# Kernel optimization log

Hardware: AMD Instinct MI355X
Metric: run time of the kernel (lower is better)

The kernel has to match this reference:

```python
import jax, jax.numpy as jnp
from jax import lax
import numpy as np

INPUT_SIZE = 300
HIDDEN = 128
NUM_CLASSES = 2
BATCH = 256
SEQ = 512


def setup_inputs() -> dict:
    key = jax.random.key(0)
    ks = jax.random.split(key, 7)
    s = 1.0 / np.sqrt(HIDDEN)
    x = jax.random.normal(ks[0], (BATCH, SEQ, INPUT_SIZE), dtype=jnp.float32)
    # PyTorch GRU parameter layout: gates stacked [reset; update; new] along dim 0
    W_ih = jax.random.uniform(ks[1], (3 * HIDDEN, INPUT_SIZE), jnp.float32, -s, s)
    W_hh = jax.random.uniform(ks[2], (3 * HIDDEN, HIDDEN), jnp.float32, -s, s)
    b_ih = jax.random.uniform(ks[3], (3 * HIDDEN,), jnp.float32, -s, s)
    b_hh = jax.random.uniform(ks[4], (3 * HIDDEN,), jnp.float32, -s, s)
    W_out = jax.random.uniform(ks[5], (NUM_CLASSES, HIDDEN), jnp.float32, -s, s)
    b_out = jax.random.uniform(ks[6], (NUM_CLASSES,), jnp.float32, -s, s)
    return {"x": x, "W_ih": W_ih, "W_hh": W_hh, "b_ih": b_ih,
            "b_hh": b_hh, "W_out": W_out, "b_out": b_out}


def reference(x, W_ih, W_hh, b_ih, b_hh, W_out, b_out):
    B, T, _ = x.shape
    H = W_hh.shape[1]
    # Precompute input-to-gate projections for all timesteps: [B, T, 3H]
    xg = jnp.einsum('bti,gi->btg', x, W_ih) + b_ih
    xg_t = jnp.swapaxes(xg, 0, 1)  # [T, B, 3H]

    def step(h, xg_step):
        hg = h @ W_hh.T + b_hh                                  # [B, 3H]
        r = jax.nn.sigmoid(xg_step[:, :H] + hg[:, :H])
        z = jax.nn.sigmoid(xg_step[:, H:2 * H] + hg[:, H:2 * H])
        n = jnp.tanh(xg_step[:, 2 * H:] + r * hg[:, 2 * H:])
        h_new = (1.0 - z) * n + z * h
        return h_new, None

    h0 = jnp.zeros((B, H), dtype=x.dtype)
    h_last, _ = lax.scan(step, h0, xg_t)
    # forward takes GRU output at last timestep -> relu -> linear -> log_softmax
    feat = jax.nn.relu(h_last)
    logits = feat @ W_out.T + b_out
    return jax.nn.log_softmax(logits, axis=1)
```

## Files before the change

### kernel.cpp

```cpp
#include <hip/hip_runtime.h>
#include <hip/hip_bf16.h>
#include <math.h>

#define BATCH 256
#define SEQ   512
#define INS   300
#define KP    320
#define HID   128
#define NG    384

typedef __attribute__((ext_vector_type(8))) short short8;
typedef __attribute__((ext_vector_type(4))) float f32x4;

__device__ __forceinline__ float bf2f(unsigned short u) {
    unsigned int v = ((unsigned int)u) << 16;
    return __uint_as_float(v);
}
__device__ __forceinline__ unsigned short f2bf(float f) {
    unsigned int u = __float_as_uint(f);
    unsigned int r = (u + 0x7FFFu + ((u >> 16) & 1u)) >> 16;
    return (unsigned short)r;
}

__global__ void conv_wih(const float* __restrict__ Wih,
                         unsigned short* __restrict__ Whi,
                         unsigned short* __restrict__ Wlo)
{
    int idx = blockIdx.x * 256 + threadIdx.x;
    if (idx >= NG * KP) return;
    int g = idx / KP, k = idx - g * KP;
    float v = (k < INS) ? Wih[g * INS + k] : 0.f;
    unsigned short h = f2bf(v);
    float r = v - bf2f(h);
    Whi[idx] = h;
    Wlo[idx] = f2bf(r);
}

template <bool BF16OUT>
__launch_bounds__(512, 2)
__global__ void xg_fused(const float* __restrict__ x,
                         const unsigned short* __restrict__ Whi,
                         const unsigned short* __restrict__ Wlo,
                         const float* __restrict__ bih,
                         void* __restrict__ xg_out,
                         int t0, int CT)
{
    __shared__ unsigned short Ah[128][40], Al[128][40];

    const int tid  = threadIdx.x;
    const int lane = tid & 63;
    const int w    = tid >> 6;
    const int wm   = (w & 1) * 64;
    const int wn   = (w >> 1) * 96;
    const int m0   = blockIdx.x * 128;

    const int srow = tid >> 2;
    const int kq   = tid & 3;
    const int rr = m0 + srow;
    const int bb = rr / CT;
    const float* xrow = x + (size_t)(bb * SEQ + t0 + (rr - bb * CT)) * INS;

    const int lmf = lane & 15;
    const int lk  = (lane >> 4) * 8;

    f32x4 acc[4][6] = {};

    float av[8];
    auto loadA = [&](int ks) {
        const int k0 = ks * 32 + kq * 8;
        if (k0 + 8 <= INS) {
            float4 f0 = *(const float4*)(xrow + k0);
            float4 f1 = *(const float4*)(xrow + k0 + 4);
            av[0] = f0.x; av[1] = f0.y; av[2] = f0.z; av[3] = f0.w;
            av[4] = f1.x; av[5] = f1.y; av[6] = f1.z; av[7] = f1.w;
        } else {
            #pragma unroll
            for (int i = 0; i < 8; i++)
                av[i] = (k0 + i < INS) ? xrow[k0 + i] : 0.f;
        }
    };
    loadA(0);

    for (int ks = 0; ks < KP / 32; ks++) {
        short8 bh[6], bl[6];
        #pragma unroll
        for (int ni = 0; ni < 6; ni++) {
            const size_t off = (size_t)(wn + ni * 16 + lmf) * KP + ks * 32 + lk;
            bh[ni] = *(const short8*)(Whi + off);
            bl[ni] = *(const short8*)(Wlo + off);
        }

        __syncthreads();
        {
            union { unsigned short us[8]; uint4 q; } ph, pl;
            #pragma unroll
            for (int i = 0; i < 8; i++) {
                unsigned short h = f2bf(av[i]);
                ph.us[i] = h;
                pl.us[i] = f2bf(av[i] - bf2f(h));
            }
            *(uint4*)&Ah[srow][kq * 8] = ph.q;
            *(uint4*)&Al[srow][kq * 8] = pl.q;
        }
        if (ks + 1 < KP / 32) loadA(ks + 1);
        __syncthreads();

        short8 ah[4], al[4];
        #pragma unroll
        for (int mi = 0; mi < 4; mi++) {
            ah[mi] = *(const short8*)&Ah[wm + mi * 16 + lmf][lk];
            al[mi] = *(const short8*)&Al[wm + mi * 16 + lmf][lk];
        }
        #pragma unroll
        for (int ni = 0; ni < 6; ni++) {
            #pragma unroll
            for (int mi = 0; mi < 4; mi++) {
                acc[mi][ni] = __builtin_amdgcn_mfma_f32_16x16x32_bf16(ah[mi], bh[ni], acc[mi][ni], 0, 0, 0);
                acc[mi][ni] = __builtin_amdgcn_mfma_f32_16x16x32_bf16(ah[mi], bl[ni], acc[mi][ni], 0, 0, 0);
                acc[mi][ni] = __builtin_amdgcn_mfma_f32_16x16x32_bf16(al[mi], bh[ni], acc[mi][ni], 0, 0, 0);
            }
        }
    }

    const int crow = (lane >> 4) * 4;
    #pragma unroll
    for (int ni = 0; ni < 6; ni++) {
        const int col = wn + ni * 16 + lmf;
        const float bias = bih[col];
        #pragma unroll
        for (int mi = 0; mi < 4; mi++) {
            #pragma unroll
            for (int i = 0; i < 4; i++) {
                const size_t row = (size_t)(m0 + wm + mi * 16 + crow + i);
                const float val = acc[mi][ni][i] + bias;
                if (BF16OUT) ((unsigned short*)xg_out)[row * NG + col] = f2bf(val);
                else         ((float*)xg_out)[row * NG + col] = val;
            }
        }
    }
}

template <bool BF16XG>
__launch_bounds__(512, 2)
__global__ void gru_mfma(const void* __restrict__ xg_in,
                         const float* __restrict__ Whh,
                         const float* __restrict__ bhh,
                         float* __restrict__ hstate,
                         int t0, int CT, int initial, int final_chunk,
                         const float* __restrict__ Wout,
                         const float* __restrict__ bout,
                         float* __restrict__ out)
{
    const int b    = blockIdx.x;
    const int tid  = threadIdx.x;
    const int w    = tid >> 6;
    const int lane = tid & 63;
    const int lm   = lane & 15;
    const int quad = lane >> 4;

    __shared__ alignas(16) unsigned short hbuf[2][2][160];
    __shared__ float red[2 * HID];

    const int mts[3] = {w, 8 + w, 16 + w};

    short8 w_hi[3][4], w_lo[3][4];
    #pragma unroll
    for (int t = 0; t < 3; t++) {
        const float* wrow = Whh + (size_t)(mts[t] * 16 + lm) * HID + quad * 8;
        #pragma unroll
        for (int kt = 0; kt < 4; kt++) {
            float4 f0 = *(const float4*)(wrow + kt * 32);
            float4 f1 = *(const float4*)(wrow + kt * 32 + 4);
            float vv[8] = {f0.x, f0.y, f0.z, f0.w, f1.x, f1.y, f1.z, f1.w};
            short8 h8, l8;
            #pragma unroll
            for (int i = 0; i < 8; i++) {
                unsigned short h = f2bf(vv[i]);
                h8[i] = (short)h;
                l8[i] = (short)f2bf(vv[i] - bf2f(h));
            }
            w_hi[t][kt] = h8;
            w_lo[t][kt] = l8;
        }
    }

    const int jd = w * 16 + lm;
    float hprev = 0.f, bhr = 0.f, bhz = 0.f, bhn = 0.f, wo0 = 0.f, wo1 = 0.f;
    float nx0r = 0.f, nx0z = 0.f, nx0n = 0.f;
    float nx1r = 0.f, nx1z = 0.f, nx1n = 0.f;
    const float* xgf = (const float*)xg_in;
    const unsigned short* xgb = (const unsigned short*)xg_in;

    if (lane < 16) {
        float h0 = initial ? 0.f : hstate[b * HID + jd];
        hprev = h0;
        bhr = bhh[jd]; bhz = bhh[HID + jd]; bhn = bhh[2 * HID + jd];
        wo0 = Wout[jd]; wo1 = Wout[HID + jd];
        unsigned short hh = f2bf(h0);
        hbuf[0][0][jd] = hh;
        hbuf[0][1][jd] = f2bf(h0 - bf2f(hh));
        const size_t nb0 = (size_t)b * CT * NG;
        const size_t nb1 = nb0 + NG;
        if (BF16XG) {
            nx0r = bf2f(xgb[nb0 + jd]); nx0z = bf2f(xgb[nb0 + HID + jd]); nx0n = bf2f(xgb[nb0 + 2 * HID + jd]);
            nx1r = bf2f(xgb[nb1 + jd]); nx1z = bf2f(xgb[nb1 + HID + jd]); nx1n = bf2f(xgb[nb1 + 2 * HID + jd]);
        } else {
            nx0r = xgf[nb0 + jd]; nx0z = xgf[nb0 + HID + jd]; nx0n = xgf[nb0 + 2 * HID + jd];
            nx1r = xgf[nb1 + jd]; nx1z = xgf[nb1 + HID + jd]; nx1n = xgf[nb1 + 2 * HID + jd];
        }
    }
    __syncthreads();

    const int psel = ((lm & 3) == 1) ? 1 : 0;

    const f32x4 z4 = {0.f, 0.f, 0.f, 0.f};

#define GRU_STEP(P, T, NXR, NXZ, NXN)                                                             \
    {                                                                                             \
        short8 a2[4];                                                                             \
        _Pragma("unroll")                                                                         \
        for (int kt = 0; kt < 4; kt++)                                                            \
            a2[kt] = *(const short8*)&hbuf[P][psel][kt * 32 + quad * 8];                          \
        f32x4 acc[3];                                                                             \
        _Pragma("unroll")                                                                         \
        for (int t = 0; t < 3; t++)                                                               \
            acc[t] = __builtin_amdgcn_mfma_f32_16x16x32_bf16(a2[0], w_hi[t][0], z4, 0, 0, 0);     \
        _Pragma("unroll")                                                                         \
        for (int kt = 1; kt < 4; kt++) {                                                          \
            _Pragma("unroll")                                                                     \
            for (int t = 0; t < 3; t++)                                                           \
                acc[t] = __builtin_amdgcn_mfma_f32_16x16x32_bf16(a2[kt], w_hi[t][kt], acc[t], 0, 0, 0); \
        }                                                                                         \
        _Pragma("unroll")                                                                         \
        for (int kt = 0; kt < 4; kt++) {                                                          \
            _Pragma("unroll")                                                                     \
            for (int t = 0; t < 3; t++)                                                           \
                acc[t] = __builtin_amdgcn_mfma_f32_16x16x32_bf16(a2[kt], w_lo[t][kt], acc[t], 0, 0, 0); \
        }                                                                                         \
        if (lane < 16) {                                                                          \
                             \
            float hgr = (acc[0][0] + acc[0][1]) + bhr;                                            \
            float hgz = (acc[1][0] + acc[1][1]) + bhz;                                            \
            float hgn = (acc[2][0] + acc[2][1]) + bhn;                                            \
            float rg = __builtin_amdgcn_rcpf(1.f + __expf(-((NXR) + hgr)));                       \
            float zg = __builtin_amdgcn_rcpf(1.f + __expf(-((NXZ) + hgz)));                       \
            float nv = (NXN) + rg * hgn;                                                          \
            float e  = __expf(2.f * nv);                                                          \
            float ng = 1.f - 2.f * __builtin_amdgcn_rcpf(e + 1.f);                                \
            hprev = (1.f - zg) * ng + zg * hprev;                                                 \
            unsigned short hh = f2bf(hprev);                                                      \
            hbuf[1 - (P)][0][jd] = hh;                                                            \
            hbuf[1 - (P)][1][jd] = f2bf(hprev - bf2f(hh));                                        \
            if ((T) + 2 < CT) {         \
                const size_t nb = ((size_t)b * CT + (T) + 2) * NG;                                \
                if (BF16XG) { NXR = bf2f(xgb[nb + jd]); NXZ = bf2f(xgb[nb + HID + jd]); NXN = bf2f(xgb[nb + 2 * HID + jd]); } \
                else        { NXR = xgf[nb + jd];       NXZ = xgf[nb + HID + jd];       NXN = xgf[nb + 2 * HID + jd]; }       \
            }                                                                                     \
        }                                                                                         \
        asm volatile("s_waitcnt lgkmcnt(0)\ns_barrier" ::: "memory");                             \
    }

    for (int tt = 0; tt < CT; tt += 2) {
        GRU_STEP(0, tt,     nx0r, nx0z, nx0n)
        GRU_STEP(1, tt + 1, nx1r, nx1z, nx1n)
    }
#undef GRU_STEP

    if (lane < 16) hstate[b * HID + jd] = hprev;

    if (final_chunk) {
        if (lane < 16) {
            float f = hprev > 0.f ? hprev : 0.f;
            red[jd] = f * wo0;
            red[HID + jd] = f * wo1;
        }
        __syncthreads();
        if (tid < 64) {
            float l0 = red[tid] + red[64 + tid];
            float l1 = red[HID + tid] + red[HID + 64 + tid];
            #pragma unroll
            for (int d = 32; d > 0; d >>= 1) {
                l0 += __shfl_down(l0, d, 64);
                l1 += __shfl_down(l1, d, 64);
            }
            if (tid == 0) {
                l0 += bout[0]; l1 += bout[1];
                float m = fmaxf(l0, l1);
                float lse = m + logf(__expf(l0 - m) + __expf(l1 - m));
                out[b * 2 + 0] = l0 - lse;
                out[b * 2 + 1] = l1 - lse;
            }
        }
    }
}

extern "C" void kernel_launch(void* const* d_in, const int* in_sizes, int n_in,
                              void* d_out, int out_size, void* d_ws, size_t ws_size,
                              hipStream_t stream) {
    const float* x    = (const float*)d_in[0];
    const float* Wih  = (const float*)d_in[1];
    const float* Whh  = (const float*)d_in[2];
    const float* bih  = (const float*)d_in[3];
    const float* bhh  = (const float*)d_in[4];
    const float* Wout = (const float*)d_in[5];
    const float* bout = (const float*)d_in[6];
    float* out = (float*)d_out;

    unsigned short* Whi = (unsigned short*)d_ws;
    unsigned short* Wlo = (unsigned short*)((char*)d_ws + 245760);
    float* hstate = (float*)((char*)d_ws + 491520);
    void*  xg     = (void*)((char*)d_ws + 622592);
    const size_t avail = ws_size > 622592 ? ws_size - 622592 : 0;

    bool bf16;
    int CT;
    if (avail >= (size_t)BATCH * SEQ * NG * 4) {
        bf16 = false; CT = SEQ;
    } else if (avail >= (size_t)BATCH * SEQ * NG * 2) {
        bf16 = true;  CT = SEQ;
    } else {
        bf16 = true;
        CT = 64;
        while (CT * 2 <= SEQ && avail >= (size_t)BATCH * (size_t)(CT * 2) * NG * 2) CT *= 2;
    }

    conv_wih<<<(NG * KP + 255) / 256, 256, 0, stream>>>(Wih, Whi, Wlo);

    for (int t0 = 0; t0 < SEQ; t0 += CT) {
        dim3 gridA((BATCH * CT) / 128);
        const int initial = (t0 == 0);
        const int final_chunk = (t0 + CT >= SEQ);
        if (bf16) {
            xg_fused<true><<<gridA, 512, 0, stream>>>(x, Whi, Wlo, bih, xg, t0, CT);
            gru_mfma<true><<<BATCH, 512, 0, stream>>>(xg, Whh, bhh, hstate, t0, CT,
                                                      initial, final_chunk, Wout, bout, out);
        } else {
            xg_fused<false><<<gridA, 512, 0, stream>>>(x, Whi, Wlo, bih, xg, t0, CT);
            gru_mfma<false><<<BATCH, 512, 0, stream>>>(xg, Whh, bhh, hstate, t0, CT,
                                                       initial, final_chunk, Wout, bout, out);
        }
    }
}
```

Baseline: 636.1 us.

## Overlap input projection with GRU recurrence via double-buffered chunked fused kernel

```diff
diff --git a/kernel.cpp b/kernel.cpp
--- a/kernel.cpp
+++ b/kernel.cpp
@@ -36,184 +36,82 @@
     Wlo[idx] = f2bf(r);
 }
 
-template <bool BF16OUT>
 __launch_bounds__(512, 2)
-__global__ void xg_fused(const float* __restrict__ x,
-                         const unsigned short* __restrict__ Whi,
-                         const unsigned short* __restrict__ Wlo,
-                         const float* __restrict__ bih,
-                         void* __restrict__ xg_out,
-                         int t0, int CT)
+__global__ void fused_pipe(const float* __restrict__ x,
+                           const unsigned short* __restrict__ Whi,
+                           const unsigned short* __restrict__ Wlo,
+                           const float* __restrict__ bih,
+                           unsigned short* __restrict__ xg_w,
+                           int t0x, int do_xg, int ctp,
+                           const unsigned short* __restrict__ xg_r,
+                           const float* __restrict__ Whh,
+                           const float* __restrict__ bhh,
+                           float* __restrict__ hstate,
+                           int initial, int final_chunk, int do_gru,
+                           const float* __restrict__ Wout,
+                           const float* __restrict__ bout,
+                           float* __restrict__ out)
 {
-    __shared__ unsigned short Ah[128][40], Al[128][40];
+    __shared__ alignas(16) unsigned char smem[10304];
 
     const int tid  = threadIdx.x;
     const int lane = tid & 63;
     const int w    = tid >> 6;
-    const int wm   = (w & 1) * 64;
-    const int wn   = (w >> 1) * 96;
-    const int m0   = blockIdx.x * 128;
-
-    const int srow = tid >> 2;
-    const int kq   = tid & 3;
-    const int rr = m0 + srow;
-    const int bb = rr / CT;
-    const float* xrow = x + (size_t)(bb * SEQ + t0 + (rr - bb * CT)) * INS;
-
-    const int lmf = lane & 15;
-    const int lk  = (lane >> 4) * 8;
-
-    f32x4 acc[4][6] = {};
-
-    float av[8];
-    auto loadA = [&](int ks) {
-        const int k0 = ks * 32 + kq * 8;
-        if (k0 + 8 <= INS) {
-            float4 f0 = *(const float4*)(xrow + k0);
-            float4 f1 = *(const float4*)(xrow + k0 + 4);
-            av[0] = f0.x; av[1] = f0.y; av[2] = f0.z; av[3] = f0.w;
-            av[4] = f1.x; av[5] = f1.y; av[6] = f1.z; av[7] = f1.w;
-        } else {
+
+    if (blockIdx.x < BATCH) {
+        if (!do_gru) return;
+        const int b    = blockIdx.x;
+        const int lm   = lane & 15;
+        const int quad = lane >> 4;
+
+        unsigned short (*hbuf)[2][160] = (unsigned short (*)[2][160])smem;
+        float* red = (float*)(smem + 1280);
+
+        const int mts[3] = {w, 8 + w, 16 + w};
+
+        short8 w_hi[3][4], w_lo[3][4];
+        #pragma unroll
+        for (int t = 0; t < 3; t++) {
+            const float* wrow = Whh + (size_t)(mts[t] * 16 + lm) * HID + quad * 8;
             #pragma unroll
-            for (int i = 0; i < 8; i++)
-                av[i] = (k0 + i < INS) ? xrow[k0 + i] : 0.f;
-        }
-    };
-    loadA(0);
-
-    for (int ks = 0; ks < KP / 32; ks++) {
-        short8 bh[6], bl[6];
-        #pragma unroll
-        for (int ni = 0; ni < 6; ni++) {
-            const size_t off = (size_t)(wn + ni * 16 + lmf) * KP + ks * 32 + lk;
-            bh[ni] = *(const short8*)(Whi + off);
-            bl[ni] = *(const short8*)(Wlo + off);
-        }
-
+            for (int kt = 0; kt < 4; kt++) {
+                float4 f0 = *(const float4*)(wrow + kt * 32);
+                float4 f1 = *(const float4*)(wrow + kt * 32 + 4);
+                float vv[8] = {f0.x, f0.y, f0.z, f0.w, f1.x, f1.y, f1.z, f1.w};
+                short8 h8, l8;
+                #pragma unroll
+                for (int i = 0; i < 8; i++) {
+                    unsigned short h = f2bf(vv[i]);
+                    h8[i] = (short)h;
+                    l8[i] = (short)f2bf(vv[i] - bf2f(h));
+                }
+                w_hi[t][kt] = h8;
+                w_lo[t][kt] = l8;
+            }
+        }
+
+        const int jd = w * 16 + lm;
+        float hprev = 0.f, bhr = 0.f, bhz = 0.f, bhn = 0.f, wo0 = 0.f, wo1 = 0.f;
+        float nx0r = 0.f, nx0z = 0.f, nx0n = 0.f;
+        float nx1r = 0.f, nx1z = 0.f, nx1n = 0.f;
+
+        if (lane < 16) {
+            float h0 = initial ? 0.f : hstate[b * HID + jd];
+            hprev = h0;
+            bhr = bhh[jd]; bhz = bhh[HID + jd]; bhn = bhh[2 * HID + jd];
+            wo0 = Wout[jd]; wo1 = Wout[HID + jd];
+            unsigned short hh = f2bf(h0);
+            hbuf[0][0][jd] = hh;
+            hbuf[0][1][jd] = f2bf(h0 - bf2f(hh));
+            const size_t nb0 = (size_t)b * ctp * NG;
+            const size_t nb1 = nb0 + NG;
+            nx0r = bf2f(xg_r[nb0 + jd]); nx0z = bf2f(xg_r[nb0 + HID + jd]); nx0n = bf2f(xg_r[nb0 + 2 * HID + jd]);
+            nx1r = bf2f(xg_r[nb1 + jd]); nx1z = bf2f(xg_r[nb1 + HID + jd]); nx1n = bf2f(xg_r[nb1 + 2 * HID + jd]);
+        }
         __syncthreads();
-        {
-            union { unsigned short us[8]; uint4 q; } ph, pl;
-            #pragma unroll
-            for (int i = 0; i < 8; i++) {
-                unsigned short h = f2bf(av[i]);
-                ph.us[i] = h;
-                pl.us[i] = f2bf(av[i] - bf2f(h));
-            }
-            *(uint4*)&Ah[srow][kq * 8] = ph.q;
-            *(uint4*)&Al[srow][kq * 8] = pl.q;
-        }
-        if (ks + 1 < KP / 32) loadA(ks + 1);
-        __syncthreads();
-
-        short8 ah[4], al[4];
-        #pragma unroll
-        for (int mi = 0; mi < 4; mi++) {
-            ah[mi] = *(const short8*)&Ah[wm + mi * 16 + lmf][lk];
-            al[mi] = *(const short8*)&Al[wm + mi * 16 + lmf][lk];
-        }
-        #pragma unroll
-        for (int ni = 0; ni < 6; ni++) {
-            #pragma unroll
-            for (int mi = 0; mi < 4; mi++) {
-                acc[mi][ni] = __builtin_amdgcn_mfma_f32_16x16x32_bf16(ah[mi], bh[ni], acc[mi][ni], 0, 0, 0);
-                acc[mi][ni] = __builtin_amdgcn_mfma_f32_16x16x32_bf16(ah[mi], bl[ni], acc[mi][ni], 0, 0, 0);
-                acc[mi][ni] = __builtin_amdgcn_mfma_f32_16x16x32_bf16(al[mi], bh[ni], acc[mi][ni], 0, 0, 0);
-            }
-        }
-    }
-
-    const int crow = (lane >> 4) * 4;
-    #pragma unroll
-    for (int ni = 0; ni < 6; ni++) {
-        const int col = wn + ni * 16 + lmf;
-        const float bias = bih[col];
-        #pragma unroll
-        for (int mi = 0; mi < 4; mi++) {
-            #pragma unroll
-            for (int i = 0; i < 4; i++) {
-                const size_t row = (size_t)(m0 + wm + mi * 16 + crow + i);
-                const float val = acc[mi][ni][i] + bias;
-                if (BF16OUT) ((unsigned short*)xg_out)[row * NG + col] = f2bf(val);
-                else         ((float*)xg_out)[row * NG + col] = val;
-            }
-        }
-    }
-}
-
-template <bool BF16XG>
-__launch_bounds__(512, 2)
-__global__ void gru_mfma(const void* __restrict__ xg_in,
-                         const float* __restrict__ Whh,
-                         const float* __restrict__ bhh,
-                         float* __restrict__ hstate,
-                         int t0, int CT, int initial, int final_chunk,
-                         const float* __restrict__ Wout,
-                         const float* __restrict__ bout,
-                         float* __restrict__ out)
-{
-    const int b    = blockIdx.x;
-    const int tid  = threadIdx.x;
-    const int w    = tid >> 6;
-    const int lane = tid & 63;
-    const int lm   = lane & 15;
-    const int quad = lane >> 4;
-
-    __shared__ alignas(16) unsigned short hbuf[2][2][160];
-    __shared__ float red[2 * HID];
-
-    const int mts[3] = {w, 8 + w, 16 + w};
-
-    short8 w_hi[3][4], w_lo[3][4];
-    #pragma unroll
-    for (int t = 0; t < 3; t++) {
-        const float* wrow = Whh + (size_t)(mts[t] * 16 + lm) * HID + quad * 8;
-        #pragma unroll
-        for (int kt = 0; kt < 4; kt++) {
-            float4 f0 = *(const float4*)(wrow + kt * 32);
-            float4 f1 = *(const float4*)(wrow + kt * 32 + 4);
-            float vv[8] = {f0.x, f0.y, f0.z, f0.w, f1.x, f1.y, f1.z, f1.w};
-            short8 h8, l8;
-            #pragma unroll
-            for (int i = 0; i < 8; i++) {
-                unsigned short h = f2bf(vv[i]);
-                h8[i] = (short)h;
-                l8[i] = (short)f2bf(vv[i] - bf2f(h));
-            }
-            w_hi[t][kt] = h8;
-            w_lo[t][kt] = l8;
-        }
-    }
-
-    const int jd = w * 16 + lm;
-    float hprev = 0.f, bhr = 0.f, bhz = 0.f, bhn = 0.f, wo0 = 0.f, wo1 = 0.f;
-    float nx0r = 0.f, nx0z = 0.f, nx0n = 0.f;
-    float nx1r = 0.f, nx1z = 0.f, nx1n = 0.f;
-    const float* xgf = (const float*)xg_in;
-    const unsigned short* xgb = (const unsigned short*)xg_in;
-
-    if (lane < 16) {
-        float h0 = initial ? 0.f : hstate[b * HID + jd];
-        hprev = h0;
-        bhr = bhh[jd]; bhz = bhh[HID + jd]; bhn = bhh[2 * HID + jd];
-        wo0 = Wout[jd]; wo1 = Wout[HID + jd];
-        unsigned short hh = f2bf(h0);
-        hbuf[0][0][jd] = hh;
-        hbuf[0][1][jd] = f2bf(h0 - bf2f(hh));
-        const size_t nb0 = (size_t)b * CT * NG;
-        const size_t nb1 = nb0 + NG;
-        if (BF16XG) {
-            nx0r = bf2f(xgb[nb0 + jd]); nx0z = bf2f(xgb[nb0 + HID + jd]); nx0n = bf2f(xgb[nb0 + 2 * HID + jd]);
-            nx1r = bf2f(xgb[nb1 + jd]); nx1z = bf2f(xgb[nb1 + HID + jd]); nx1n = bf2f(xgb[nb1 + 2 * HID + jd]);
-        } else {
-            nx0r = xgf[nb0 + jd]; nx0z = xgf[nb0 + HID + jd]; nx0n = xgf[nb0 + 2 * HID + jd];
-            nx1r = xgf[nb1 + jd]; nx1z = xgf[nb1 + HID + jd]; nx1n = xgf[nb1 + 2 * HID + jd];
-        }
-    }
-    __syncthreads();
-
-    const int psel = ((lm & 3) == 1) ? 1 : 0;
-
-    const f32x4 z4 = {0.f, 0.f, 0.f, 0.f};
+
+        const int psel = ((lm & 3) == 1) ? 1 : 0;
+        const f32x4 z4 = {0.f, 0.f, 0.f, 0.f};
 
 #define GRU_STEP(P, T, NXR, NXZ, NXN)                                                             \
     {                                                                                             \
@@ -238,7 +136,6 @@
                 acc[t] = __builtin_amdgcn_mfma_f32_16x16x32_bf16(a2[kt], w_lo[t][kt], acc[t], 0, 0, 0); \
         }                                                                                         \
         if (lane < 16) {                                                                          \
-                             \
             float hgr = (acc[0][0] + acc[0][1]) + bhr;                                            \
             float hgz = (acc[1][0] + acc[1][1]) + bhz;                                            \
             float hgn = (acc[2][0] + acc[2][1]) + bhn;                                            \
@@ -251,44 +148,131 @@
             unsigned short hh = f2bf(hprev);                                                      \
             hbuf[1 - (P)][0][jd] = hh;                                                            \
             hbuf[1 - (P)][1][jd] = f2bf(hprev - bf2f(hh));                                        \
-            if ((T) + 2 < CT) {         \
-                const size_t nb = ((size_t)b * CT + (T) + 2) * NG;                                \
-                if (BF16XG) { NXR = bf2f(xgb[nb + jd]); NXZ = bf2f(xgb[nb + HID + jd]); NXN = bf2f(xgb[nb + 2 * HID + jd]); } \
-                else        { NXR = xgf[nb + jd];       NXZ = xgf[nb + HID + jd];       NXN = xgf[nb + 2 * HID + jd]; }       \
+            if ((T) + 2 < ctp) {        \
+                const size_t nb = ((size_t)b * ctp + (T) + 2) * NG;                               \
+                NXR = bf2f(xg_r[nb + jd]); NXZ = bf2f(xg_r[nb + HID + jd]); NXN = bf2f(xg_r[nb + 2 * HID + jd]); \
             }                                                                                     \
         }                                                                                         \
         asm volatile("s_waitcnt lgkmcnt(0)\ns_barrier" ::: "memory");                             \
     }
 
-    for (int tt = 0; tt < CT; tt += 2) {
-        GRU_STEP(0, tt,     nx0r, nx0z, nx0n)
-        GRU_STEP(1, tt + 1, nx1r, nx1z, nx1n)
-    }
+        for (int tt = 0; tt < ctp; tt += 2) {
+            GRU_STEP(0, tt,     nx0r, nx0z, nx0n)
+            GRU_STEP(1, tt + 1, nx1r, nx1z, nx1n)
+        }
 #undef GRU_STEP
 
-    if (lane < 16) hstate[b * HID + jd] = hprev;
-
-    if (final_chunk) {
-        if (lane < 16) {
-            float f = hprev > 0.f ? hprev : 0.f;
-            red[jd] = f * wo0;
-            red[HID + jd] = f * wo1;
-        }
-        __syncthreads();
-        if (tid < 64) {
-            float l0 = red[tid] + red[64 + tid];
-            float l1 = red[HID + tid] + red[HID + 64 + tid];
+        if (lane < 16) hstate[b * HID + jd] = hprev;
+
+        if (final_chunk) {
+            if (lane < 16) {
+                float f = hprev > 0.f ? hprev : 0.f;
+                red[jd] = f * wo0;
+                red[HID + jd] = f * wo1;
+            }
+            __syncthreads();
+            if (tid < 64) {
+                float l0 = red[tid] + red[64 + tid];
+                float l1 = red[HID + tid] + red[HID + 64 + tid];
+                #pragma unroll
+                for (int d = 32; d > 0; d >>= 1) {
+                    l0 += __shfl_down(l0, d, 64);
+                    l1 += __shfl_down(l1, d, 64);
+                }
+                if (tid == 0) {
+                    l0 += bout[0]; l1 += bout[1];
+                    float m = fmaxf(l0, l1);
+                    float lse = m + logf(__expf(l0 - m) + __expf(l1 - m));
+                    out[b * 2 + 0] = l0 - lse;
+                    out[b * 2 + 1] = l1 - lse;
+                }
+            }
+        }
+    } else {
+        if (!do_xg) return;
+        const int xb = blockIdx.x - BATCH;
+        if (xb >= (BATCH * ctp) / 64) return;
+
+        unsigned short (*Ah)[40] = (unsigned short (*)[40])smem;
+        unsigned short (*Al)[40] = (unsigned short (*)[40])(smem + 5120);
+
+        const int wm = (w & 1) * 32;
+        const int wn = (w >> 1) * 96;
+        const int m0 = xb * 64;
+
+        const int srow = tid >> 3;
+        const int kq   = tid & 7;
+        const int rr = m0 + srow;
+        const int bb = rr / ctp;
+        const float* xrow = x + (size_t)(bb * SEQ + t0x + (rr - bb * ctp)) * INS;
+
+        const int lmf = lane & 15;
+        const int lk  = (lane >> 4) * 8;
+
+        f32x4 acc[2][6] = {};
+
+        float av[4];
+        auto loadA = [&](int ks) {
+            const int k0 = ks * 32 + kq * 4;
+            if (k0 + 4 <= INS) {
+                float4 f = *(const float4*)(xrow + k0);
+                av[0] = f.x; av[1] = f.y; av[2] = f.z; av[3] = f.w;
+            } else {
+                #pragma unroll
+                for (int i = 0; i < 4; i++)
+                    av[i] = (k0 + i < INS) ? xrow[k0 + i] : 0.f;
+            }
+        };
+        loadA(0);
+
+        for (int ks = 0; ks < KP / 32; ks++) {
+            __syncthreads();
+            {
+                union { unsigned short us[4]; uint2 q; } ph, pl;
+                #pragma unroll
+                for (int i = 0; i < 4; i++) {
+                    unsigned short h = f2bf(av[i]);
+                    ph.us[i] = h;
+                    pl.us[i] = f2bf(av[i] - bf2f(h));
+                }
+                *(uint2*)&Ah[srow][kq * 4] = ph.q;
+                *(uint2*)&Al[srow][kq * 4] = pl.q;
+            }
+            if (ks + 1 < KP / 32) loadA(ks + 1);
+            __syncthreads();
+
+            short8 ah[2], al[2];
             #pragma unroll
-            for (int d = 32; d > 0; d >>= 1) {
-                l0 += __shfl_down(l0, d, 64);
-                l1 += __shfl_down(l1, d, 64);
-            }
-            if (tid == 0) {
-                l0 += bout[0]; l1 += bout[1];
-                float m = fmaxf(l0, l1);
-                float lse = m + logf(__expf(l0 - m) + __expf(l1 - m));
-                out[b * 2 + 0] = l0 - lse;
-                out[b * 2 + 1] = l1 - lse;
+            for (int mi = 0; mi < 2; mi++) {
+                ah[mi] = *(const short8*)&Ah[wm + mi * 16 + lmf][lk];
+                al[mi] = *(const short8*)&Al[wm + mi * 16 + lmf][lk];
+            }
+            #pragma unroll
+            for (int ni = 0; ni < 6; ni++) {
+                const size_t off = (size_t)(wn + ni * 16 + lmf) * KP + ks * 32 + lk;
+                short8 bh = *(const short8*)(Whi + off);
+                short8 bl = *(const short8*)(Wlo + off);
+                #pragma unroll
+                for (int mi = 0; mi < 2; mi++) {
+                    acc[mi][ni] = __builtin_amdgcn_mfma_f32_16x16x32_bf16(ah[mi], bh, acc[mi][ni], 0, 0, 0);
+                    acc[mi][ni] = __builtin_amdgcn_mfma_f32_16x16x32_bf16(ah[mi], bl, acc[mi][ni], 0, 0, 0);
+                    acc[mi][ni] = __builtin_amdgcn_mfma_f32_16x16x32_bf16(al[mi], bh, acc[mi][ni], 0, 0, 0);
+                }
+            }
+        }
+
+        const int crow = (lane >> 4) * 4;
+        #pragma unroll
+        for (int ni = 0; ni < 6; ni++) {
+            const int col = wn + ni * 16 + lmf;
+            const float bias = bih[col];
+            #pragma unroll
+            for (int mi = 0; mi < 2; mi++) {
+                #pragma unroll
+                for (int i = 0; i < 4; i++) {
+                    const size_t row = (size_t)(m0 + wm + mi * 16 + crow + i);
+                    xg_w[row * NG + col] = f2bf(acc[mi][ni][i] + bias);
+                }
             }
         }
     }
@@ -309,35 +293,26 @@
     unsigned short* Whi = (unsigned short*)d_ws;
     unsigned short* Wlo = (unsigned short*)((char*)d_ws + 245760);
     float* hstate = (float*)((char*)d_ws + 491520);
-    void*  xg     = (void*)((char*)d_ws + 622592);
+    char*  xgbase = (char*)d_ws + 622592;
     const size_t avail = ws_size > 622592 ? ws_size - 622592 : 0;
 
-    bool bf16;
-    int CT;
-    if (avail >= (size_t)BATCH * SEQ * NG * 4) {
-        bf16 = false; CT = SEQ;
-    } else if (avail >= (size_t)BATCH * SEQ * NG * 2) {
-        bf16 = true;  CT = SEQ;
-    } else {
-        bf16 = true;
-        CT = 64;
-        while (CT * 2 <= SEQ && avail >= (size_t)BATCH * (size_t)(CT * 2) * NG * 2) CT *= 2;
+    int ctp = 128;
+    while (ctp > 4 && avail < 2 * (size_t)BATCH * ctp * NG * 2) ctp >>= 1;
+    const size_t cbytes = (size_t)BATCH * ctp * NG * 2;
+    unsigned short* bufs[2] = {(unsigned short*)xgbase, (unsigned short*)(xgbase + cbytes)};
+    const int nch = SEQ / ctp;
+    const int grid = BATCH + (BATCH * ctp) / 64;
+
+    conv_wih<<<(NG * KP + 255) / 256, 256, 0, stream>>>(Wih, Whi, Wlo);
+
+    for (int k = 0; k <= nch; k++) {
+        const int do_xg  = (k < nch);
+        const int do_gru = (k >= 1);
+        fused_pipe<<<grid, 512, 0, stream>>>(
+            x, Whi, Wlo, bih,
+            bufs[k & 1], k * ctp, do_xg, ctp,
+            bufs[(k - 1) & 1], Whh, bhh, hstate,
+            (k == 1), (k == nch), do_gru,
+            Wout, bout, out);
     }
-
-    conv_wih<<<(NG * KP + 255) / 256, 256, 0, stream>>>(Wih, Whi, Wlo);
-
-    for (int t0 = 0; t0 < SEQ; t0 += CT) {
-        dim3 gridA((BATCH * CT) / 128);
-        const int initial = (t0 == 0);
-        const int final_chunk = (t0 + CT >= SEQ);
-        if (bf16) {
-            xg_fused<true><<<gridA, 512, 0, stream>>>(x, Whi, Wlo, bih, xg, t0, CT);
-            gru_mfma<true><<<BATCH, 512, 0, stream>>>(xg, Whh, bhh, hstate, t0, CT,
-                                                      initial, final_chunk, Wout, bout, out);
-        } else {
-            xg_fused<false><<<gridA, 512, 0, stream>>>(x, Whi, Wlo, bih, xg, t0, CT);
-            gru_mfma<false><<<BATCH, 512, 0, stream>>>(xg, Whh, bhh, hstate, t0, CT,
-                                                       initial, final_chunk, Wout, bout, out);
-        }
-    }
-}
+}
```

After: 880.2 us. 1.38x slower.
